# Kernel tuning notes

Hardware: AMD Instinct MI355X
Metric: run time of the kernel (lower is better)

Reference implementation:

```python
import jax, jax.numpy as jnp
import numpy as np

EPS = 1e-5


def _cbr(z, W, bn, relu=True):
    # z: [b, Cin, L]; W: [Cout, Cin]; bn: [4, Cout] = (gamma, beta, mean, var)
    # 1x1 Conv2d (bias=False) over a [b, Cin, L, 1] tensor == channel matmul.
    y = jnp.einsum('oi,bil->bol', W, z)
    g, b_, m, v = bn[0], bn[1], bn[2], bn[3]
    y = g[:, None] * (y - m[:, None]) * jax.lax.rsqrt(v[:, None] + EPS) + b_[:, None]
    return jax.nn.relu(y) if relu else y


def setup_inputs() -> dict:
    key = jax.random.key(0)
    ks = jax.random.split(key, 13)
    b, c, h, w = 32, 512, 48, 48
    in_spatial = h * w          # 2304
    inter_spatial = in_spatial // 4  # 576
    inter_channel = c // 4      # 128
    ncc = 1 + inter_channel     # 129
    return {
        'x': jax.random.normal(ks[0], (b, c, h, w), jnp.float32),
        'W_theta': jax.random.normal(ks[1], (inter_spatial, in_spatial), jnp.float32) * 0.02,
        'bn_theta': jax.random.uniform(ks[2], (4, inter_spatial), jnp.float32),
        'W_phi': jax.random.normal(ks[3], (inter_spatial, in_spatial), jnp.float32) * 0.02,
        'bn_phi': jax.random.uniform(ks[4], (4, inter_spatial), jnp.float32),
        'W_gx': jax.random.normal(ks[5], (inter_spatial, in_spatial), jnp.float32) * 0.02,
        'bn_gx': jax.random.uniform(ks[6], (4, inter_spatial), jnp.float32),
        'W_gg': jax.random.normal(ks[7], (inter_channel, 2 * c), jnp.float32) * 0.02,
        'bn_gg': jax.random.uniform(ks[8], (4, inter_channel), jnp.float32),
        'W_c1': jax.random.normal(ks[9], (ncc // 2, ncc), jnp.float32) * 0.02,
        'bn_c1': jax.random.uniform(ks[10], (4, ncc // 2), jnp.float32),
        'W_c2': jax.random.normal(ks[11], (1, ncc // 2), jnp.float32) * 0.02,
        'bn_c2': jax.random.uniform(ks[12], (4, 1), jnp.float32),
    }


def reference(x, W_theta, bn_theta, W_phi, bn_phi, W_gx, bn_gx,
              W_gg, bn_gg, W_c1, bn_c1, W_c2, bn_c2):
    b, c, h, w = x.shape
    xc = x.reshape(b, c, h * w).transpose(0, 2, 1)          # [b, hw, c]
    xc1 = _cbr(xc, W_theta, bn_theta).transpose(0, 2, 1)    # [b, c, is]
    xc2 = _cbr(xc, W_phi, bn_phi)                           # [b, is, c]
    Gc = jnp.einsum('bcs,bsd->bcd', xc1, xc2)               # [b, c, c]
    Gc_joint = jnp.concatenate([Gc.transpose(0, 2, 1), Gc], axis=1)  # [b, 2c, c]
    Gc_joint = _cbr(Gc_joint, W_gg, bn_gg)                  # [b, ic, c]
    g_xc = _cbr(xc, W_gx, bn_gx).mean(axis=1, keepdims=True)  # [b, 1, c]
    yc = jnp.concatenate([g_xc, Gc_joint], axis=1)          # [b, 1+ic, c]
    wy = _cbr(yc, W_c1, bn_c1)
    wy = _cbr(wy, W_c2, bn_c2, relu=False)                  # [b, 1, c]
    gate = jax.nn.sigmoid(wy)[:, 0, :, None, None]          # [b, c, 1, 1]
    return gate * x + x
```

## Files before the change

kernel.cpp:

```cpp
#include <hip/hip_runtime.h>
#include <cstdint>

#define EPSV 1e-5f
typedef unsigned short u16;
typedef __attribute__((ext_vector_type(8))) short bh8;
typedef __attribute__((ext_vector_type(4))) float f4;

__device__ __forceinline__ float bf2f(u16 h) { return __uint_as_float((unsigned)h << 16); }
__device__ __forceinline__ u16 f2bf(float x) {
    unsigned u = __float_as_uint(x);
    u += 0x7fffu + ((u >> 16) & 1u);
    return (u16)(u >> 16);
}

__device__ __forceinline__ void gl16(const void* g, const void* s) {
    __builtin_amdgcn_global_load_lds(
        reinterpret_cast<const __attribute__((address_space(1))) void*>((uintptr_t)g),
        reinterpret_cast<__attribute__((address_space(3))) void*>((unsigned)(uintptr_t)s),
        16, 0, 0);
}

__device__ __forceinline__ void core2(
    const u16* __restrict__ Ah, const u16* __restrict__ Al,
    const u16* __restrict__ Bh, const u16* __restrict__ Bl,
    long ldA, long ldB, int K, int rowA0, int rowB0,
    u16* lds, f4 acc[4][4])
{
    const int tid = threadIdx.x, l = tid & 63, w = tid >> 6;
    const int wr = w >> 1, wc = w & 1;
    const int srow = tid >> 2;
    const int schunk = ((tid & 3) ^ ((tid >> 3) & 3)) << 3;
    const size_t aoff = (size_t)(rowA0 + srow) * ldA + schunk;
    const size_t boff = (size_t)(rowB0 + srow) * ldB + schunk;
    const size_t a64 = (size_t)64 * ldA, b64 = (size_t)64 * ldB;
    const int rr = l & 15, cq = l >> 4;
    const int roff = rr * 64 + (((cq ^ ((rr >> 1) & 3))) << 4);
    char* const base0 = (char*)lds;
    char* const base1 = (char*)lds + 32768;
    const int nt = K >> 5;

#define STAGE_SWZ(base, s0) do { \
    gl16(Ah + aoff + (s0),       (base) +         w * 1024); \
    gl16(Ah + aoff + a64 + (s0), (base) +  4096 + w * 1024); \
    gl16(Al + aoff + (s0),       (base) +  8192 + w * 1024); \
    gl16(Al + aoff + a64 + (s0), (base) + 12288 + w * 1024); \
    gl16(Bh + boff + (s0),       (base) + 16384 + w * 1024); \
    gl16(Bh + boff + b64 + (s0), (base) + 20480 + w * 1024); \
    gl16(Bl + boff + (s0),       (base) + 24576 + w * 1024); \
    gl16(Bl + boff + b64 + (s0), (base) + 28672 + w * 1024); \
} while (0)

    STAGE_SWZ(base0, 0);
    __syncthreads();
    int p = 0;
    for (int t = 0; t < nt; ++t) {
        if (t + 1 < nt) STAGE_SWZ(p ? base0 : base1, (size_t)(t + 1) << 5);
        const char* buf = p ? base1 : base0;
        bh8 a_h[4], a_l[4], b_h[4], b_l[4];
#pragma unroll
        for (int i = 0; i < 4; ++i) {
            a_h[i] = *(const bh8*)(buf + (wr * 4 + i) * 1024 + roff);
            a_l[i] = *(const bh8*)(buf + 8192 + (wr * 4 + i) * 1024 + roff);
            b_h[i] = *(const bh8*)(buf + 16384 + (wc * 4 + i) * 1024 + roff);
            b_l[i] = *(const bh8*)(buf + 24576 + (wc * 4 + i) * 1024 + roff);
        }
#pragma unroll
        for (int i = 0; i < 4; ++i)
#pragma unroll
            for (int j = 0; j < 4; ++j)
                acc[i][j] = __builtin_amdgcn_mfma_f32_16x16x32_bf16(a_h[i], b_h[j], acc[i][j], 0, 0, 0);
#pragma unroll
        for (int i = 0; i < 4; ++i)
#pragma unroll
            for (int j = 0; j < 4; ++j)
                acc[i][j] = __builtin_amdgcn_mfma_f32_16x16x32_bf16(a_h[i], b_l[j], acc[i][j], 0, 0, 0);
#pragma unroll
        for (int i = 0; i < 4; ++i)
#pragma unroll
            for (int j = 0; j < 4; ++j)
                acc[i][j] = __builtin_amdgcn_mfma_f32_16x16x32_bf16(a_l[i], b_h[j], acc[i][j], 0, 0, 0);
        __syncthreads();
        p ^= 1;
    }
#undef STAGE_SWZ
}

__global__ __launch_bounds__(512) void gemm_s1_v6(
    const u16* __restrict__ Xh, const u16* __restrict__ Xl,
    const u16* __restrict__ W0h, const u16* __restrict__ W0l,
    const u16* __restrict__ W1h, const u16* __restrict__ W1l,
    const u16* __restrict__ W2h, const u16* __restrict__ W2l,
    const float* __restrict__ bn0, const float* __restrict__ bn1,
    const float* __restrict__ bn2,
    u16* __restrict__ Y0h, u16* __restrict__ Y0l,
    u16* __restrict__ Y1h, u16* __restrict__ Y1l,
    u16* __restrict__ Y2h, u16* __restrict__ Y2l)
{
    const int h = blockIdx.x;
    const int orig = (h & 7) * 120 + (h >> 3);
    const int ow = orig % 15;
    const int rest = orig / 15;
    const int ct = rest & 1, bz = rest >> 1;
    const int wi = ow / 5, otw = ow % 5;
    const bool full = (wi != 0);

    const u16* Bh = wi == 0 ? W0h : wi == 1 ? W1h : W2h;
    const u16* Bl = wi == 0 ? W0l : wi == 1 ? W1l : W2l;
    const float* bnp = wi == 0 ? bn0 : wi == 1 ? bn1 : bn2;
    u16* Yh = wi == 0 ? Y0h : wi == 1 ? Y1h : Y2h;
    u16* Yl = wi == 0 ? Y0l : wi == 1 ? Y1l : Y2l;

    __shared__ u16 lds[73728];

    const int tid = threadIdx.x, l = tid & 63, w = tid >> 6;
    const int wm = w >> 1, wn = w & 1;
    const int srow = tid >> 2;
    const int schunk = ((tid & 3) ^ ((tid >> 3) & 3)) << 3;
    const long ldK = 2304;
    const int rowA0 = bz * 512 + ct * 256;
    const int rowB0 = otw * 128;
    const size_t aoff = (size_t)(rowA0 + srow) * ldK + schunk;
    const size_t boff = (size_t)(rowB0 + srow) * ldK + schunk;
    const size_t a128 = (size_t)128 * ldK;
    const int rr = l & 15, cq = l >> 4;
    const int roff = rr * 64 + ((cq ^ ((rr >> 1) & 3)) << 4);
    char* const ldsb = (char*)lds;
    const int nt = 72;

#define ST_AHI(sb, s0) do { \
    gl16(Xh + aoff + (s0),        (sb) +         w * 1024); \
    gl16(Xh + aoff + a128 + (s0), (sb) +  8192 + w * 1024); } while (0)
#define ST_ALO(sb, s0) do { \
    gl16(Xl + aoff + (s0),        (sb) + 16384 + w * 1024); \
    gl16(Xl + aoff + a128 + (s0), (sb) + 24576 + w * 1024); } while (0)
#define ST_BHI(sb, s0) gl16(Bh + boff + (s0), (sb) + 32768 + w * 1024)
#define ST_BLO(sb, s0) gl16(Bl + boff + (s0), (sb) + 40960 + w * 1024)

    f4 acc[4][4];
    const f4 z4 = {0.f, 0.f, 0.f, 0.f};
#pragma unroll
    for (int i = 0; i < 4; ++i)
#pragma unroll
        for (int j = 0; j < 4; ++j) acc[i][j] = z4;

    ST_AHI(ldsb, 0); if (full) ST_ALO(ldsb, 0); ST_BHI(ldsb, 0); ST_BLO(ldsb, 0);
    ST_AHI(ldsb + 49152, 32); if (full) ST_ALO(ldsb + 49152, 32);
    ST_BHI(ldsb + 49152, 32); ST_BLO(ldsb + 49152, 32);
    if (full) asm volatile("s_waitcnt vmcnt(6)" ::: "memory");
    else      asm volatile("s_waitcnt vmcnt(4)" ::: "memory");
    __builtin_amdgcn_sched_barrier(0);
    __builtin_amdgcn_s_barrier();

    for (int t = 0; t < nt; ++t) {
        const char* buf = ldsb + (t % 3) * 49152;
        char* sbuf = ldsb + ((t + 2) % 3) * 49152;
        const bool pre = (t + 2 < nt);
        const int s0 = (t + 2) << 5;

        bh8 a_h[4], b_h[4], a_l[4], b_l[4];
#pragma unroll
        for (int i = 0; i < 4; ++i)
            a_h[i] = *(const bh8*)(buf + (wm * 4 + i) * 1024 + roff);
#pragma unroll
        for (int j = 0; j < 4; ++j)
            b_h[j] = *(const bh8*)(buf + 32768 + (wn * 4 + j) * 1024 + roff);
        if (pre) ST_AHI(sbuf, s0);
        __builtin_amdgcn_s_barrier();
        __builtin_amdgcn_s_setprio(1);
#pragma unroll
        for (int i = 0; i < 4; ++i)
#pragma unroll
            for (int j = 0; j < 4; ++j)
                acc[i][j] = __builtin_amdgcn_mfma_f32_16x16x32_bf16(a_h[i], b_h[j], acc[i][j], 0, 0, 0);
        __builtin_amdgcn_s_setprio(0);
        __builtin_amdgcn_s_barrier();
        if (full) {
#pragma unroll
            for (int i = 0; i < 4; ++i)
                a_l[i] = *(const bh8*)(buf + 16384 + (wm * 4 + i) * 1024 + roff);
        }
#pragma unroll
        for (int j = 0; j < 4; ++j)
            b_l[j] = *(const bh8*)(buf + 40960 + (wn * 4 + j) * 1024 + roff);
        if (pre) { if (full) ST_ALO(sbuf, s0); ST_BHI(sbuf, s0); }
        __builtin_amdgcn_s_barrier();
        __builtin_amdgcn_s_setprio(1);
#pragma unroll
        for (int i = 0; i < 4; ++i)
#pragma unroll
            for (int j = 0; j < 4; ++j)
                acc[i][j] = __builtin_amdgcn_mfma_f32_16x16x32_bf16(a_h[i], b_l[j], acc[i][j], 0, 0, 0);
        __builtin_amdgcn_s_setprio(0);
        __builtin_amdgcn_s_barrier();
        if (pre) ST_BLO(sbuf, s0);
        if (t + 1 < nt) {
            if (pre) {
                if (full) asm volatile("s_waitcnt vmcnt(6)" ::: "memory");
                else      asm volatile("s_waitcnt vmcnt(4)" ::: "memory");
            } else {
                asm volatile("s_waitcnt vmcnt(0)" ::: "memory");
            }
            __builtin_amdgcn_sched_barrier(0);
        }
        __builtin_amdgcn_s_barrier();
        if (full) {
            __builtin_amdgcn_s_setprio(1);
#pragma unroll
            for (int i = 0; i < 4; ++i)
#pragma unroll
                for (int j = 0; j < 4; ++j)
                    acc[i][j] = __builtin_amdgcn_mfma_f32_16x16x32_bf16(a_l[i], b_h[j], acc[i][j], 0, 0, 0);
            __builtin_amdgcn_s_setprio(0);
        }
        __builtin_amdgcn_s_barrier();
    }
#undef ST_AHI
#undef ST_ALO
#undef ST_BHI
#undef ST_BLO

    const int mb = ct * 256 + wm * 64;
    const int nbw = otw * 128 + wn * 64;
    const int lm = l & 15;
#pragma unroll
    for (int j = 0; j < 4; ++j) {
        const int o = nbw + j * 16 + lm;
        const bool val = (o < 576);
        float sc = 0.f, sh = 0.f;
        if (val) {
            const float gg = bnp[o], be = bnp[576 + o], mm = bnp[1152 + o], vv = bnp[1728 + o];
            sc = gg * rsqrtf(vv + EPSV);
            sh = be - mm * sc;
        }
#pragma unroll
        for (int i = 0; i < 4; ++i) {
            const int c = mb + i * 16 + ((l >> 4) << 2);
#pragma unroll
            for (int r = 0; r < 4; ++r) {
                const float y = val ? fmaxf(acc[i][j][r] * sc + sh, 0.f) : 0.f;
                const u16 hh = f2bf(y);
                const u16 lo = f2bf(y - bf2f(hh));
                const size_t off = ((size_t)bz * 512 + c + r) * 640 + o;
                Yh[off] = hh; Yl[off] = lo;
            }
        }
    }
}

__global__ __launch_bounds__(256) void gemm_u(
    const u16* __restrict__ Wggh, const u16* __restrict__ Wggl,
    const u16* __restrict__ tnth, const u16* __restrict__ tntl,
    const u16* __restrict__ pnth, const u16* __restrict__ pntl,
    u16* __restrict__ U1h, u16* __restrict__ U1l,
    u16* __restrict__ U2h, u16* __restrict__ U2l)
{
    const int h = blockIdx.x;
    const int orig = (h & 7) * 40 + (h >> 3);
    const int ot = orig % 5;
    const int rest = orig / 5;
    const int u = rest & 1, b = rest >> 1;

    const u16* Ah = Wggh + (u ? 512 : 0);
    const u16* Al = Wggl + (u ? 512 : 0);
    const u16* Bh = u ? tnth : pnth;
    const u16* Bl = u ? tntl : pntl;

    __shared__ u16 lds[32768];
    f4 acc[4][4];
    const f4 z4 = {0.f, 0.f, 0.f, 0.f};
#pragma unroll
    for (int i = 0; i < 4; ++i)
#pragma unroll
        for (int j = 0; j < 4; ++j) acc[i][j] = z4;

    core2(Ah, Al, Bh, Bl, 1024, 512, 512, 0, b * 640 + ot * 128, lds, acc);

    u16* Uh = u ? U2h : U1h;
    u16* Ul = u ? U2l : U1l;
    const int l = threadIdx.x & 63, w = threadIdx.x >> 6;
    const int wr = w >> 1, wc = w & 1;
#pragma unroll
    for (int i = 0; i < 4; ++i)
#pragma unroll
        for (int j = 0; j < 4; ++j)
#pragma unroll
            for (int r = 0; r < 4; ++r) {
                const int irow = wr * 64 + i * 16 + ((l >> 4) << 2) + r;
                const int ocol = ot * 128 + wc * 64 + j * 16 + (l & 15);
                const float v = acc[i][j][r];
                const u16 hh = f2bf(v);
                const u16 lo = f2bf(v - bf2f(hh));
                const size_t off = ((size_t)b * 128 + irow) * 640 + ocol;
                Uh[off] = hh; Ul[off] = lo;
            }
}

__global__ __launch_bounds__(256) void gemm_term_p(
    const u16* __restrict__ U1h, const u16* __restrict__ U1l,
    const u16* __restrict__ U2h, const u16* __restrict__ U2l,
    const u16* __restrict__ tth, const u16* __restrict__ ttl,
    const u16* __restrict__ pth, const u16* __restrict__ ptl,
    float* __restrict__ GGa, float* __restrict__ GGb)
{
    const int h = blockIdx.x;
    const int orig = (h & 7) * 32 + (h >> 3);
    const int dt = orig & 3;
    const int u = (orig >> 2) & 1;
    const int b = orig >> 3;

    const u16* Ah = u ? U2h : U1h;
    const u16* Al = u ? U2l : U1l;
    const u16* Bh = u ? pth : tth;
    const u16* Bl = u ? ptl : ttl;
    float* G = u ? GGb : GGa;

    __shared__ u16 lds[32768];
    f4 acc[4][4];
    const f4 z4 = {0.f, 0.f, 0.f, 0.f};
#pragma unroll
    for (int i = 0; i < 4; ++i)
#pragma unroll
        for (int j = 0; j < 4; ++j) acc[i][j] = z4;

    core2(Ah, Al, Bh, Bl, 640, 640, 640,
          b * 128, b * 512 + dt * 128, lds, acc);

    const int l = threadIdx.x & 63, w = threadIdx.x >> 6;
    const int wr = w >> 1, wc = w & 1;
#pragma unroll
    for (int i = 0; i < 4; ++i)
#pragma unroll
        for (int j = 0; j < 4; ++j)
#pragma unroll
            for (int r = 0; r < 4; ++r) {
                const int irow = wr * 64 + i * 16 + ((l >> 4) << 2) + r;
                const int dcol = dt * 128 + wc * 64 + j * 16 + (l & 15);
                G[((size_t)b * 128 + irow) * 512 + dcol] = acc[i][j][r];
            }
}

__global__ __launch_bounds__(256) void gg_combine(
    float* __restrict__ GGa, const float* __restrict__ GGb,
    const float* __restrict__ bn, long n4)
{
    const long i = (long)blockIdx.x * 256 + threadIdx.x;
    if (i >= n4) return;
    const int irow = (int)((i >> 7) & 127);
    const float g = bn[irow], be = bn[128 + irow], m = bn[256 + irow], v = bn[384 + irow];
    const float sc = g * rsqrtf(v + EPSV);
    const float sh = be - m * sc;
    float4 a = ((const float4*)GGa)[i];
    const float4 b = ((const float4*)GGb)[i];
    a.x = fmaxf((a.x + b.x) * sc + sh, 0.f);
    a.y = fmaxf((a.y + b.y) * sc + sh, 0.f);
    a.z = fmaxf((a.z + b.z) * sc + sh, 0.f);
    a.w = fmaxf((a.w + b.w) * sc + sh, 0.f);
    ((float4*)GGa)[i] = a;
}

__global__ __launch_bounds__(256) void transpose_y(
    const u16* __restrict__ s0, u16* __restrict__ d0,
    const u16* __restrict__ s1, u16* __restrict__ d1,
    const u16* __restrict__ s2, u16* __restrict__ d2,
    const u16* __restrict__ s3, u16* __restrict__ d3)
{
    const int pz = blockIdx.z;
    const int b = pz >> 2, pl = pz & 3;
    const u16* src = pl == 0 ? s0 : pl == 1 ? s1 : pl == 2 ? s2 : s3;
    u16* dst = pl == 0 ? d0 : pl == 1 ? d1 : pl == 2 ? d2 : d3;
    const int o0 = blockIdx.x * 64, c0 = blockIdx.y * 64;
    __shared__ u16 t[64][72];
    const int tid = threadIdx.x;
#pragma unroll
    for (int rdx = tid; rdx < 512; rdx += 256) {
        const int c = rdx >> 3, oc = (rdx & 7) << 3;
        *(bh8*)&t[c][oc] = *(const bh8*)&src[((size_t)b * 512 + c0 + c) * 640 + o0 + oc];
    }
    __syncthreads();
#pragma unroll
    for (int wdx = tid; wdx < 512; wdx += 256) {
        const int o = wdx >> 3, cc = (wdx & 7) << 3;
        u16 v[8];
#pragma unroll
        for (int e = 0; e < 8; ++e) v[e] = t[cc + e][o];
        *(bh8*)&dst[((size_t)b * 640 + o0 + o) * 512 + c0 + cc] = *(bh8*)&v[0];
    }
}

__global__ __launch_bounds__(256) void conv_split(
    const float* __restrict__ in, u16* __restrict__ hi, u16* __restrict__ lo, long n8)
{
    long i = (long)blockIdx.x * 256 + threadIdx.x;
    const long stride = (long)gridDim.x * 256;
    for (; i < n8; i += stride) {
        const float4 a = ((const float4*)in)[2 * i];
        const float4 b = ((const float4*)in)[2 * i + 1];
        const float v[8] = {a.x, a.y, a.z, a.w, b.x, b.y, b.z, b.w};
        unsigned hw[4], lw[4];
#pragma unroll
        for (int k = 0; k < 4; ++k) {
            const u16 h0 = f2bf(v[2 * k]), h1 = f2bf(v[2 * k + 1]);
            const u16 l0 = f2bf(v[2 * k] - bf2f(h0)), l1 = f2bf(v[2 * k + 1] - bf2f(h1));
            hw[k] = (unsigned)h0 | ((unsigned)h1 << 16);
            lw[k] = (unsigned)l0 | ((unsigned)l1 << 16);
        }
        *(uint4*)&hi[8 * i] = make_uint4(hw[0], hw[1], hw[2], hw[3]);
        *(uint4*)&lo[8 * i] = make_uint4(lw[0], lw[1], lw[2], lw[3]);
    }
}

__global__ __launch_bounds__(256) void conv_w_pad(
    const float* __restrict__ W, u16* __restrict__ hi, u16* __restrict__ lo,
    int rows, long n8)
{
    const long i = (long)blockIdx.x * 256 + threadIdx.x;
    if (i >= n8) return;
    const long e = i * 8;
    const int row = (int)(e / 2304);
    unsigned hw[4] = {0, 0, 0, 0}, lw[4] = {0, 0, 0, 0};
    if (row < rows) {
        const float4 a = ((const float4*)W)[2 * i];
        const float4 b = ((const float4*)W)[2 * i + 1];
        const float v[8] = {a.x, a.y, a.z, a.w, b.x, b.y, b.z, b.w};
#pragma unroll
        for (int k = 0; k < 4; ++k) {
            const u16 h0 = f2bf(v[2 * k]), h1 = f2bf(v[2 * k + 1]);
            const u16 l0 = f2bf(v[2 * k] - bf2f(h0)), l1 = f2bf(v[2 * k + 1] - bf2f(h1));
            hw[k] = (unsigned)h0 | ((unsigned)h1 << 16);
            lw[k] = (unsigned)l0 | ((unsigned)l1 << 16);
        }
    }
    *(uint4*)&hi[8 * i] = make_uint4(hw[0], hw[1], hw[2], hw[3]);
    *(uint4*)&lo[8 * i] = make_uint4(lw[0], lw[1], lw[2], lw[3]);
}

__global__ __launch_bounds__(256) void row_mean(
    const u16* __restrict__ Yh, const u16* __restrict__ Yl,
    float* __restrict__ out, int rows)
{
    const int l = threadIdx.x & 63;
    const int row = blockIdx.x * 4 + (threadIdx.x >> 6);
    if (row >= rows) return;
    const u16* ph = Yh + (size_t)row * 640;
    const u16* pl = Yl + (size_t)row * 640;
    float s = 0.f;
    struct U8 { u16 u[8]; };
    for (int k = l; k < 80; k += 64) {
        const U8 a = *(const U8*)&ph[k * 8];
        const U8 b = *(const U8*)&pl[k * 8];
#pragma unroll
        for (int e = 0; e < 8; ++e) s += bf2f(a.u[e]) + bf2f(b.u[e]);
    }
    for (int off = 32; off; off >>= 1) s += __shfl_down(s, off, 64);
    if (l == 0) out[row] = s * (1.f / 576.f);
}

__global__ __launch_bounds__(256)
void gate_kernel(const float* __restrict__ gxc, const float* __restrict__ GG,
                 const float* __restrict__ Wc1, const float* __restrict__ bn1,
                 const float* __restrict__ Wc2, const float* __restrict__ bn2,
                 float* __restrict__ gate, int IC, int D, int OC)
{
    const int b  = blockIdx.y;
    const int d0 = blockIdx.x * 64;

    __shared__ float yc_s[129][64];
    __shared__ float part[4][64];

    const int tid = threadIdx.x;
    for (int idx = tid; idx < 129 * 64; idx += 256) {
        const int j = idx >> 6, d = idx & 63;
        yc_s[j][d] = (j == 0) ? gxc[b * D + d0 + d]
                              : GG[((size_t)b * IC + (j - 1)) * D + d0 + d];
    }
    __syncthreads();

    const int d = tid & 63;
    const int q = tid >> 6;
    float acc2 = 0.f;
    for (int o = q * 16; o < q * 16 + 16; ++o) {
        float s = 0.f;
        const float* __restrict__ w = &Wc1[o * 129];
        for (int j = 0; j < 129; ++j) s = fmaf(w[j], yc_s[j][d], s);
        const float g1 = bn1[o], be1 = bn1[OC + o], m1 = bn1[2 * OC + o], v1 = bn1[3 * OC + o];
        const float sc = g1 / sqrtf(v1 + EPSV);
        const float w1 = fmaxf(s * sc + (be1 - m1 * sc), 0.f);
        acc2 = fmaf(Wc2[o], w1, acc2);
    }
    part[q][d] = acc2;
    __syncthreads();
    if (q == 0) {
        const float s = part[0][d] + part[1][d] + part[2][d] + part[3][d];
        const float g2 = bn2[0], be2 = bn2[1], m2 = bn2[2], v2 = bn2[3];
        const float sc = g2 / sqrtf(v2 + EPSV);
        const float wy = s * sc + (be2 - m2 * sc);
        gate[b * D + d0 + d] = 1.f / (1.f + expf(-wy));
    }
}

__global__ __launch_bounds__(256)
void final_kernel(const float* __restrict__ x, const float* __restrict__ gate,
                  float* __restrict__ out, long n4, int sp4)
{
    long i = (long)blockIdx.x * blockDim.x + threadIdx.x;
    const long stride = (long)gridDim.x * blockDim.x;
    for (; i < n4; i += stride) {
        float4 v = ((const float4*)x)[i];
        const long bc = i / sp4;
        const float gm = 1.f + gate[bc];
        v.x *= gm; v.y *= gm; v.z *= gm; v.w *= gm;
        ((float4*)out)[i] = v;
    }
}

extern "C" void kernel_launch(void* const* d_in, const int* in_sizes, int n_in,
                              void* d_out, int out_size, void* d_ws, size_t ws_size,
                              hipStream_t stream)
{
    const float* x        = (const float*)d_in[0];
    const float* W_theta  = (const float*)d_in[1];
    const float* bn_theta = (const float*)d_in[2];
    const float* W_phi    = (const float*)d_in[3];
    const float* bn_phi   = (const float*)d_in[4];
    const float* W_gx     = (const float*)d_in[5];
    const float* bn_gx    = (const float*)d_in[6];
    const float* W_gg     = (const float*)d_in[7];
    const float* bn_gg    = (const float*)d_in[8];
    const float* W_c1     = (const float*)d_in[9];
    const float* bn_c1    = (const float*)d_in[10];
    const float* W_c2     = (const float*)d_in[11];
    const float* bn_c2    = (const float*)d_in[12];
    float* out = (float*)d_out;

    const int B = 32, C = 512, S = 2304, O = 576, OP = 640, IC = 128, OC = 64;
    const size_t P  = (size_t)B * C * OP;
    const size_t WP = (size_t)OP * S;
    const size_t UP = (size_t)B * IC * OP;

    u16* tth = (u16*)d_out;
    u16* ttl = tth + P;
    u16* pth = ttl + P;
    u16* ptl = pth + P;
    u16* Wgh = ptl + P;
    u16* Wgl = Wgh + WP;
    u16* Wth = Wgl + WP;
    u16* Wtl = Wth + WP;
    u16* Wph = Wtl + WP;
    u16* Wpl = Wph + WP;
    u16* wggh = Wpl + WP;
    u16* wggl = wggh + (size_t)IC * 1024;
    u16* u1h = wggl + (size_t)IC * 1024;
    u16* u1l = u1h + UP;
    u16* u2h = u1l + UP;
    u16* u2l = u2h + UP;
    float* GGa = (float*)(u2l + UP);
    float* GGb = GGa + (size_t)B * IC * C;

    u16* Xhi  = (u16*)d_ws;
    u16* Xlo  = Xhi + (size_t)B * C * S;
    u16* ygxh = Xlo + (size_t)B * C * S;
    u16* ygxl = ygxh + P;
    float* gxc  = (float*)(ygxl + P);
    float* gate = gxc + (size_t)B * C;
    u16* tnth = (u16*)d_ws;
    u16* tntl = tnth + P;
    u16* pnth = tntl + P;
    u16* pntl = pnth + P;

    const dim3 blk(256);

    const long wN8 = (long)WP / 8;
    conv_w_pad<<<dim3((unsigned)(wN8 / 256)), blk, 0, stream>>>(W_gx,    Wgh, Wgl, O, wN8);
    conv_w_pad<<<dim3((unsigned)(wN8 / 256)), blk, 0, stream>>>(W_theta, Wth, Wtl, O, wN8);
    conv_w_pad<<<dim3((unsigned)(wN8 / 256)), blk, 0, stream>>>(W_phi,   Wph, Wpl, O, wN8);
    conv_split<<<dim3(64), blk, 0, stream>>>(W_gg, wggh, wggl, (long)IC * 1024 / 8);

    conv_split<<<dim3(2048), blk, 0, stream>>>(x, Xhi, Xlo, (long)B * C * S / 8);
    gemm_s1_v6<<<dim3(960), dim3(512), 0, stream>>>(
        Xhi, Xlo, Wgh, Wgl, Wth, Wtl, Wph, Wpl,
        bn_gx, bn_theta, bn_phi,
        ygxh, ygxl, tth, ttl, pth, ptl);
    row_mean<<<dim3(4096), blk, 0, stream>>>(ygxh, ygxl, gxc, B * C);

    transpose_y<<<dim3(10, 8, 128), blk, 0, stream>>>(
        tth, tnth, ttl, tntl, pth, pnth, ptl, pntl);

    gemm_u<<<dim3(320), blk, 0, stream>>>(wggh, wggl, tnth, tntl, pnth, pntl,
                                          u1h, u1l, u2h, u2l);

    gemm_term_p<<<dim3(256), blk, 0, stream>>>(u1h, u1l, u2h, u2l,
                                               tth, ttl, pth, ptl, GGa, GGb);
    gg_combine<<<dim3(2048), blk, 0, stream>>>(GGa, GGb, bn_gg,
                                               (long)B * IC * C / 4);

    gate_kernel<<<dim3(C / 64, B), blk, 0, stream>>>(gxc, GGa, W_c1, bn_c1, W_c2, bn_c2,
                                                     gate, IC, C, OC);

    final_kernel<<<dim3(2048), blk, 0, stream>>>(x, gate, out,
                                                 (long)B * C * S / 4, S / 4);
}
```

Measured before the change: 633.2 us.

## Fuse fp32-to-bf16 hi/lo split of x into the stage-1 GEMM loads

Drops the separate conv_split pass over x and has the stage-1 GEMM stream fp32 x straight into LDS. Each tile is split into bf16 hi/lo pairs in registers right after the LDS read. This removes one full read and two half-size writes of the 151 MB input, plus a kernel launch. In exchange the GEMM moves twice the A bytes per tile (fp32 instead of bf16), and every block redundantly recomputes the split. The non-full (wi==0) blocks now also load the low-part data volume.

```diff
diff --git a/kernel.cpp b/kernel.cpp
--- a/kernel.cpp
+++ b/kernel.cpp
@@ -18,6 +18,25 @@
         reinterpret_cast<const __attribute__((address_space(1))) void*>((uintptr_t)g),
         reinterpret_cast<__attribute__((address_space(3))) void*>((unsigned)(uintptr_t)s),
         16, 0, 0);
+}
+
+__device__ __forceinline__ void split8(const f4 va, const f4 vb,
+                                       bh8* hi, bh8* lo, bool needLo)
+{
+    union U { bh8 v; u16 u[8]; };
+    U H, L;
+#pragma unroll
+    for (int e = 0; e < 4; ++e) {
+        const float x0 = va[e], x1 = vb[e];
+        const u16 h0 = f2bf(x0), h1 = f2bf(x1);
+        H.u[e] = h0; H.u[e + 4] = h1;
+        if (needLo) {
+            L.u[e]     = f2bf(x0 - bf2f(h0));
+            L.u[e + 4] = f2bf(x1 - bf2f(h1));
+        }
+    }
+    *hi = H.v;
+    if (needLo) *lo = L.v;
 }
 
 __device__ __forceinline__ void core2(
@@ -85,8 +104,8 @@
 #undef STAGE_SWZ
 }
 
-__global__ __launch_bounds__(512) void gemm_s1_v6(
-    const u16* __restrict__ Xh, const u16* __restrict__ Xl,
+__global__ __launch_bounds__(512) void gemm_s1_v7(
+    const float* __restrict__ Xf,
     const u16* __restrict__ W0h, const u16* __restrict__ W0l,
     const u16* __restrict__ W1h, const u16* __restrict__ W1l,
     const u16* __restrict__ W2h, const u16* __restrict__ W2l,
@@ -114,25 +133,30 @@
 
     const int tid = threadIdx.x, l = tid & 63, w = tid >> 6;
     const int wm = w >> 1, wn = w & 1;
-    const int srow = tid >> 2;
-    const int schunk = ((tid & 3) ^ ((tid >> 3) & 3)) << 3;
     const long ldK = 2304;
     const int rowA0 = bz * 512 + ct * 256;
     const int rowB0 = otw * 128;
-    const size_t aoff = (size_t)(rowA0 + srow) * ldK + schunk;
+
+    const int arow = tid >> 3;
+    const int acd  = (tid & 7) ^ (arow & 7);
+    const size_t aoffF = (size_t)(rowA0 + arow) * ldK + acd * 4;
+    const int srow = tid >> 2;
+    const int schunk = ((tid & 3) ^ ((tid >> 3) & 3)) << 3;
     const size_t boff = (size_t)(rowB0 + srow) * ldK + schunk;
-    const size_t a128 = (size_t)128 * ldK;
+
     const int rr = l & 15, cq = l >> 4;
-    const int roff = rr * 64 + ((cq ^ ((rr >> 1) & 3)) << 4);
+    const int roffB = rr * 64 + ((cq ^ ((rr >> 1) & 3)) << 4);
+    const int slot1 = (2 * cq) ^ (rr & 7);
+    const int roffA1 = rr * 128 + (slot1 << 4);
+    const int roffA2 = rr * 128 + ((slot1 ^ 1) << 4);
     char* const ldsb = (char*)lds;
     const int nt = 72;
 
-#define ST_AHI(sb, s0) do { \
-    gl16(Xh + aoff + (s0),        (sb) +         w * 1024); \
-    gl16(Xh + aoff + a128 + (s0), (sb) +  8192 + w * 1024); } while (0)
-#define ST_ALO(sb, s0) do { \
-    gl16(Xl + aoff + (s0),        (sb) + 16384 + w * 1024); \
-    gl16(Xl + aoff + a128 + (s0), (sb) + 24576 + w * 1024); } while (0)
+#define ST_A(sb, s0) do { \
+    gl16(Xf + aoffF + (s0),          (sb) +         w * 1024); \
+    gl16(Xf + aoffF + 147456 + (s0), (sb) +  8192 + w * 1024); \
+    gl16(Xf + aoffF + 294912 + (s0), (sb) + 16384 + w * 1024); \
+    gl16(Xf + aoffF + 442368 + (s0), (sb) + 24576 + w * 1024); } while (0)
 #define ST_BHI(sb, s0) gl16(Bh + boff + (s0), (sb) + 32768 + w * 1024)
 #define ST_BLO(sb, s0) gl16(Bl + boff + (s0), (sb) + 40960 + w * 1024)
 
@@ -143,11 +167,9 @@
 #pragma unroll
         for (int j = 0; j < 4; ++j) acc[i][j] = z4;
 
-    ST_AHI(ldsb, 0); if (full) ST_ALO(ldsb, 0); ST_BHI(ldsb, 0); ST_BLO(ldsb, 0);
-    ST_AHI(ldsb + 49152, 32); if (full) ST_ALO(ldsb + 49152, 32);
-    ST_BHI(ldsb + 49152, 32); ST_BLO(ldsb + 49152, 32);
-    if (full) asm volatile("s_waitcnt vmcnt(6)" ::: "memory");
-    else      asm volatile("s_waitcnt vmcnt(4)" ::: "memory");
+    ST_A(ldsb, 0); ST_BHI(ldsb, 0); ST_BLO(ldsb, 0);
+    ST_A(ldsb + 49152, 32); ST_BHI(ldsb + 49152, 32); ST_BLO(ldsb + 49152, 32);
+    asm volatile("s_waitcnt vmcnt(6)" ::: "memory");
     __builtin_amdgcn_sched_barrier(0);
     __builtin_amdgcn_s_barrier();
 
@@ -157,14 +179,18 @@
         const bool pre = (t + 2 < nt);
         const int s0 = (t + 2) << 5;
 
-        bh8 a_h[4], b_h[4], a_l[4], b_l[4];
-#pragma unroll
-        for (int i = 0; i < 4; ++i)
-            a_h[i] = *(const bh8*)(buf + (wm * 4 + i) * 1024 + roff);
+        if (pre) ST_A(sbuf, s0);
+        bh8 a_h[4], a_l[4], b_h[4], b_l[4];
+#pragma unroll
+        for (int i = 0; i < 4; ++i) {
+            const int fb = (wm * 64 + i * 16) * 128;
+            const f4 va = *(const f4*)(buf + fb + roffA1);
+            const f4 vb = *(const f4*)(buf + fb + roffA2);
+            split8(va, vb, &a_h[i], &a_l[i], full);
+        }
 #pragma unroll
         for (int j = 0; j < 4; ++j)
-            b_h[j] = *(const bh8*)(buf + 32768 + (wn * 4 + j) * 1024 + roff);
-        if (pre) ST_AHI(sbuf, s0);
+            b_h[j] = *(const bh8*)(buf + 32768 + (wn * 4 + j) * 1024 + roffB);
         __builtin_amdgcn_s_barrier();
         __builtin_amdgcn_s_setprio(1);
 #pragma unroll
@@ -174,15 +200,10 @@
                 acc[i][j] = __builtin_amdgcn_mfma_f32_16x16x32_bf16(a_h[i], b_h[j], acc[i][j], 0, 0, 0);
         __builtin_amdgcn_s_setprio(0);
         __builtin_amdgcn_s_barrier();
-        if (full) {
-#pragma unroll
-            for (int i = 0; i < 4; ++i)
-                a_l[i] = *(const bh8*)(buf + 16384 + (wm * 4 + i) * 1024 + roff);
-        }
+        if (pre) ST_BHI(sbuf, s0);
 #pragma unroll
         for (int j = 0; j < 4; ++j)
-            b_l[j] = *(const bh8*)(buf + 40960 + (wn * 4 + j) * 1024 + roff);
-        if (pre) { if (full) ST_ALO(sbuf, s0); ST_BHI(sbuf, s0); }
+            b_l[j] = *(const bh8*)(buf + 40960 + (wn * 4 + j) * 1024 + roffB);
         __builtin_amdgcn_s_barrier();
         __builtin_amdgcn_s_setprio(1);
 #pragma unroll
@@ -194,12 +215,8 @@
         __builtin_amdgcn_s_barrier();
         if (pre) ST_BLO(sbuf, s0);
         if (t + 1 < nt) {
-            if (pre) {
-                if (full) asm volatile("s_waitcnt vmcnt(6)" ::: "memory");
-                else      asm volatile("s_waitcnt vmcnt(4)" ::: "memory");
-            } else {
-                asm volatile("s_waitcnt vmcnt(0)" ::: "memory");
-            }
+            if (pre) asm volatile("s_waitcnt vmcnt(6)" ::: "memory");
+            else     asm volatile("s_waitcnt vmcnt(0)" ::: "memory");
             __builtin_amdgcn_sched_barrier(0);
         }
         __builtin_amdgcn_s_barrier();
@@ -214,8 +231,7 @@
         }
         __builtin_amdgcn_s_barrier();
     }
-#undef ST_AHI
-#undef ST_ALO
+#undef ST_A
 #undef ST_BHI
 #undef ST_BLO
 
@@ -556,16 +572,14 @@
     float* GGa = (float*)(u2l + UP);
     float* GGb = GGa + (size_t)B * IC * C;
 
-    u16* Xhi  = (u16*)d_ws;
-    u16* Xlo  = Xhi + (size_t)B * C * S;
-    u16* ygxh = Xlo + (size_t)B * C * S;
-    u16* ygxl = ygxh + P;
-    float* gxc  = (float*)(ygxl + P);
-    float* gate = gxc + (size_t)B * C;
     u16* tnth = (u16*)d_ws;
     u16* tntl = tnth + P;
     u16* pnth = tntl + P;
     u16* pntl = pnth + P;
+    u16* ygxh = pntl + P;
+    u16* ygxl = ygxh + P;
+    float* gxc  = (float*)(ygxl + P);
+    float* gate = gxc + (size_t)B * C;
 
     const dim3 blk(256);
 
@@ -575,9 +589,8 @@
     conv_w_pad<<<dim3((unsigned)(wN8 / 256)), blk, 0, stream>>>(W_phi,   Wph, Wpl, O, wN8);
     conv_split<<<dim3(64), blk, 0, stream>>>(W_gg, wggh, wggl, (long)IC * 1024 / 8);
 
-    conv_split<<<dim3(2048), blk, 0, stream>>>(x, Xhi, Xlo, (long)B * C * S / 8);
-    gemm_s1_v6<<<dim3(960), dim3(512), 0, stream>>>(
-        Xhi, Xlo, Wgh, Wgl, Wth, Wtl, Wph, Wpl,
+    gemm_s1_v7<<<dim3(960), dim3(512), 0, stream>>>(
+        x, Wgh, Wgl, Wth, Wtl, Wph, Wpl,
         bn_gx, bn_theta, bn_phi,
         ygxh, ygxl, tth, ttl, pth, ptl);
     row_mean<<<dim3(4096), blk, 0, stream>>>(ygxh, ygxl, gxc, B * C);
```

New measurement: 908.9 us. +43.5%, slower.

## Fuse g_x row mean into GEMM epilogue and gg_combine into gate kernel

Applied to the files above, without the earlier changes.

The g_x branch of the big GEMM now reduces its BN+ReLU output across the tile's output columns in registers and LDS and writes per-tile partial row sums, instead of storing the full hi/lo bf16 matrix and running a separate row_mean kernel. The GGa+GGb combine with BN+ReLU moves into gate_kernel's load loop, which also sums the five partial means. The three weight conversion launches are merged into one 2D grid. This removes a large intermediate write/read and several launches, at the cost of extra epilogue syncs and shuffles in the GEMM.

```diff
diff --git a/kernel.cpp b/kernel.cpp
--- a/kernel.cpp
+++ b/kernel.cpp
@@ -85,14 +85,14 @@
 #undef STAGE_SWZ
 }
 
-__global__ __launch_bounds__(512) void gemm_s1_v6(
+__global__ __launch_bounds__(512) void gemm_s1_v6b(
     const u16* __restrict__ Xh, const u16* __restrict__ Xl,
     const u16* __restrict__ W0h, const u16* __restrict__ W0l,
     const u16* __restrict__ W1h, const u16* __restrict__ W1l,
     const u16* __restrict__ W2h, const u16* __restrict__ W2l,
     const float* __restrict__ bn0, const float* __restrict__ bn1,
     const float* __restrict__ bn2,
-    u16* __restrict__ Y0h, u16* __restrict__ Y0l,
+    float* __restrict__ gxc_part,
     u16* __restrict__ Y1h, u16* __restrict__ Y1l,
     u16* __restrict__ Y2h, u16* __restrict__ Y2l)
 {
@@ -107,23 +107,23 @@
     const u16* Bh = wi == 0 ? W0h : wi == 1 ? W1h : W2h;
     const u16* Bl = wi == 0 ? W0l : wi == 1 ? W1l : W2l;
     const float* bnp = wi == 0 ? bn0 : wi == 1 ? bn1 : bn2;
-    u16* Yh = wi == 0 ? Y0h : wi == 1 ? Y1h : Y2h;
-    u16* Yl = wi == 0 ? Y0l : wi == 1 ? Y1l : Y2l;
+    u16* Yh = wi == 1 ? Y1h : Y2h;
+    u16* Yl = wi == 1 ? Y1l : Y2l;
 
     __shared__ u16 lds[73728];
 
     const int tid = threadIdx.x, l = tid & 63, w = tid >> 6;
     const int wm = w >> 1, wn = w & 1;
-    const int srow = tid >> 2;
-    const int schunk = ((tid & 3) ^ ((tid >> 3) & 3)) << 3;
     const long ldK = 2304;
     const int rowA0 = bz * 512 + ct * 256;
     const int rowB0 = otw * 128;
+    const int srow = tid >> 2;
+    const int schunk = ((tid & 3) ^ ((tid >> 3) & 3)) << 3;
     const size_t aoff = (size_t)(rowA0 + srow) * ldK + schunk;
     const size_t boff = (size_t)(rowB0 + srow) * ldK + schunk;
     const size_t a128 = (size_t)128 * ldK;
-    const int rr = l & 15, cq = l >> 4;
-    const int roff = rr * 64 + ((cq ^ ((rr >> 1) & 3)) << 4);
+    const int rr = l & 15, cq2 = l >> 4;
+    const int roff = rr * 64 + ((cq2 ^ ((rr >> 1) & 3)) << 4);
     char* const ldsb = (char*)lds;
     const int nt = 72;
 
@@ -221,27 +221,66 @@
 
     const int mb = ct * 256 + wm * 64;
     const int nbw = otw * 128 + wn * 64;
-    const int lm = l & 15;
-#pragma unroll
-    for (int j = 0; j < 4; ++j) {
-        const int o = nbw + j * 16 + lm;
-        const bool val = (o < 576);
-        float sc = 0.f, sh = 0.f;
-        if (val) {
-            const float gg = bnp[o], be = bnp[576 + o], mm = bnp[1152 + o], vv = bnp[1728 + o];
-            sc = gg * rsqrtf(vv + EPSV);
-            sh = be - mm * sc;
-        }
-#pragma unroll
-        for (int i = 0; i < 4; ++i) {
-            const int c = mb + i * 16 + ((l >> 4) << 2);
+    const int lm = l & 15, cq = l >> 4;
+
+    if (wi == 0) {
+        float rs[4][4] = {};
+#pragma unroll
+        for (int j = 0; j < 4; ++j) {
+            const int o = nbw + j * 16 + lm;
+            const bool val = (o < 576);
+            float sc = 0.f, sh = 0.f;
+            if (val) {
+                const float gg = bnp[o], be = bnp[576 + o], mm = bnp[1152 + o], vv = bnp[1728 + o];
+                sc = gg * rsqrtf(vv + EPSV);
+                sh = be - mm * sc;
+            }
+#pragma unroll
+            for (int i = 0; i < 4; ++i)
+#pragma unroll
+                for (int r = 0; r < 4; ++r)
+                    rs[i][r] += val ? fmaxf(acc[i][j][r] * sc + sh, 0.f) : 0.f;
+        }
+        __syncthreads();
+        float* ldsF = (float*)lds;
+#pragma unroll
+        for (int i = 0; i < 4; ++i)
 #pragma unroll
             for (int r = 0; r < 4; ++r) {
-                const float y = val ? fmaxf(acc[i][j][r] * sc + sh, 0.f) : 0.f;
-                const u16 hh = f2bf(y);
-                const u16 lo = f2bf(y - bf2f(hh));
-                const size_t off = ((size_t)bz * 512 + c + r) * 640 + o;
-                Yh[off] = hh; Yl[off] = lo;
+                float v = rs[i][r];
+                v += __shfl_xor(v, 1, 64);
+                v += __shfl_xor(v, 2, 64);
+                v += __shfl_xor(v, 4, 64);
+                v += __shfl_xor(v, 8, 64);
+                if (lm == 0)
+                    ldsF[wn * 256 + wm * 64 + i * 16 + cq * 4 + r] = v;
+            }
+        __syncthreads();
+        if (tid < 256)
+            gxc_part[(size_t)otw * 16384 + (size_t)bz * 512 + ct * 256 + tid]
+                = ldsF[tid] + ldsF[256 + tid];
+    } else {
+#pragma unroll
+        for (int j = 0; j < 4; ++j) {
+            const int o = nbw + j * 16 + lm;
+            const bool val = (o < 576);
+            float sc = 0.f, sh = 0.f;
+            if (val) {
+                const float gg = bnp[o], be = bnp[576 + o], mm = bnp[1152 + o], vv = bnp[1728 + o];
+                sc = gg * rsqrtf(vv + EPSV);
+                sh = be - mm * sc;
+            }
+#pragma unroll
+            for (int i = 0; i < 4; ++i) {
+                const int c = mb + i * 16 + (cq << 2);
+#pragma unroll
+                for (int r = 0; r < 4; ++r) {
+                    const float y = val ? fmaxf(acc[i][j][r] * sc + sh, 0.f) : 0.f;
+                    const u16 hh = f2bf(y);
+                    const u16 lo = f2bf(y - bf2f(hh));
+                    const size_t off = ((size_t)bz * 512 + c + r) * 640 + o;
+                    Yh[off] = hh; Yl[off] = lo;
+                }
             }
         }
     }
@@ -339,25 +378,6 @@
             }
 }
 
-__global__ __launch_bounds__(256) void gg_combine(
-    float* __restrict__ GGa, const float* __restrict__ GGb,
-    const float* __restrict__ bn, long n4)
-{
-    const long i = (long)blockIdx.x * 256 + threadIdx.x;
-    if (i >= n4) return;
-    const int irow = (int)((i >> 7) & 127);
-    const float g = bn[irow], be = bn[128 + irow], m = bn[256 + irow], v = bn[384 + irow];
-    const float sc = g * rsqrtf(v + EPSV);
-    const float sh = be - m * sc;
-    float4 a = ((const float4*)GGa)[i];
-    const float4 b = ((const float4*)GGb)[i];
-    a.x = fmaxf((a.x + b.x) * sc + sh, 0.f);
-    a.y = fmaxf((a.y + b.y) * sc + sh, 0.f);
-    a.z = fmaxf((a.z + b.z) * sc + sh, 0.f);
-    a.w = fmaxf((a.w + b.w) * sc + sh, 0.f);
-    ((float4*)GGa)[i] = a;
-}
-
 __global__ __launch_bounds__(256) void transpose_y(
     const u16* __restrict__ s0, u16* __restrict__ d0,
     const u16* __restrict__ s1, u16* __restrict__ d1,
@@ -409,10 +429,19 @@
     }
 }
 
-__global__ __launch_bounds__(256) void conv_w_pad(
-    const float* __restrict__ W, u16* __restrict__ hi, u16* __restrict__ lo,
+__global__ __launch_bounds__(256) void conv_w_pad3(
+    const float* __restrict__ Wg, const float* __restrict__ Wt,
+    const float* __restrict__ Wp,
+    u16* __restrict__ Hg, u16* __restrict__ Lg,
+    u16* __restrict__ Ht, u16* __restrict__ Lt,
+    u16* __restrict__ Hp, u16* __restrict__ Lp,
     int rows, long n8)
 {
+    const int wsel = blockIdx.y;
+    const float* W = wsel == 0 ? Wg : wsel == 1 ? Wt : Wp;
+    u16* hi = wsel == 0 ? Hg : wsel == 1 ? Ht : Hp;
+    u16* lo = wsel == 0 ? Lg : wsel == 1 ? Lt : Lp;
+
     const long i = (long)blockIdx.x * 256 + threadIdx.x;
     if (i >= n8) return;
     const long e = i * 8;
@@ -434,29 +463,10 @@
     *(uint4*)&lo[8 * i] = make_uint4(lw[0], lw[1], lw[2], lw[3]);
 }
 
-__global__ __launch_bounds__(256) void row_mean(
-    const u16* __restrict__ Yh, const u16* __restrict__ Yl,
-    float* __restrict__ out, int rows)
-{
-    const int l = threadIdx.x & 63;
-    const int row = blockIdx.x * 4 + (threadIdx.x >> 6);
-    if (row >= rows) return;
-    const u16* ph = Yh + (size_t)row * 640;
-    const u16* pl = Yl + (size_t)row * 640;
-    float s = 0.f;
-    struct U8 { u16 u[8]; };
-    for (int k = l; k < 80; k += 64) {
-        const U8 a = *(const U8*)&ph[k * 8];
-        const U8 b = *(const U8*)&pl[k * 8];
-#pragma unroll
-        for (int e = 0; e < 8; ++e) s += bf2f(a.u[e]) + bf2f(b.u[e]);
-    }
-    for (int off = 32; off; off >>= 1) s += __shfl_down(s, off, 64);
-    if (l == 0) out[row] = s * (1.f / 576.f);
-}
-
 __global__ __launch_bounds__(256)
-void gate_kernel(const float* __restrict__ gxc, const float* __restrict__ GG,
+void gate_kernel(const float* __restrict__ gxp,
+                 const float* __restrict__ GGa, const float* __restrict__ GGb,
+                 const float* __restrict__ bngg,
                  const float* __restrict__ Wc1, const float* __restrict__ bn1,
                  const float* __restrict__ Wc2, const float* __restrict__ bn2,
                  float* __restrict__ gate, int IC, int D, int OC)
@@ -470,8 +480,23 @@
     const int tid = threadIdx.x;
     for (int idx = tid; idx < 129 * 64; idx += 256) {
         const int j = idx >> 6, d = idx & 63;
-        yc_s[j][d] = (j == 0) ? gxc[b * D + d0 + d]
-                              : GG[((size_t)b * IC + (j - 1)) * D + d0 + d];
+        float v;
+        if (j == 0) {
+            float s = 0.f;
+#pragma unroll
+            for (int t = 0; t < 5; ++t)
+                s += gxp[(size_t)t * 16384 + (size_t)b * 512 + d0 + d];
+            v = s * (1.f / 576.f);
+        } else {
+            const int i = j - 1;
+            const float g = bngg[i], be = bngg[128 + i];
+            const float m = bngg[256 + i], vv = bngg[384 + i];
+            const float sc = g * rsqrtf(vv + EPSV);
+            const float sh = be - m * sc;
+            const size_t o = ((size_t)b * IC + i) * D + d0 + d;
+            v = fmaxf((GGa[o] + GGb[o]) * sc + sh, 0.f);
+        }
+        yc_s[j][d] = v;
     }
     __syncthreads();
 
@@ -558,29 +583,25 @@
 
     u16* Xhi  = (u16*)d_ws;
     u16* Xlo  = Xhi + (size_t)B * C * S;
-    u16* ygxh = Xlo + (size_t)B * C * S;
-    u16* ygxl = ygxh + P;
-    float* gxc  = (float*)(ygxl + P);
-    float* gate = gxc + (size_t)B * C;
     u16* tnth = (u16*)d_ws;
     u16* tntl = tnth + P;
     u16* pnth = tntl + P;
     u16* pntl = pnth + P;
+    float* gxc_part = (float*)(Xlo + (size_t)B * C * S);
+    float* gate = gxc_part + (size_t)5 * B * C;
 
     const dim3 blk(256);
 
     const long wN8 = (long)WP / 8;
-    conv_w_pad<<<dim3((unsigned)(wN8 / 256)), blk, 0, stream>>>(W_gx,    Wgh, Wgl, O, wN8);
-    conv_w_pad<<<dim3((unsigned)(wN8 / 256)), blk, 0, stream>>>(W_theta, Wth, Wtl, O, wN8);
-    conv_w_pad<<<dim3((unsigned)(wN8 / 256)), blk, 0, stream>>>(W_phi,   Wph, Wpl, O, wN8);
+    conv_w_pad3<<<dim3((unsigned)(wN8 / 256), 3), blk, 0, stream>>>(
+        W_gx, W_theta, W_phi, Wgh, Wgl, Wth, Wtl, Wph, Wpl, O, wN8);
     conv_split<<<dim3(64), blk, 0, stream>>>(W_gg, wggh, wggl, (long)IC * 1024 / 8);
 
     conv_split<<<dim3(2048), blk, 0, stream>>>(x, Xhi, Xlo, (long)B * C * S / 8);
-    gemm_s1_v6<<<dim3(960), dim3(512), 0, stream>>>(
+    gemm_s1_v6b<<<dim3(960), dim3(512), 0, stream>>>(
         Xhi, Xlo, Wgh, Wgl, Wth, Wtl, Wph, Wpl,
         bn_gx, bn_theta, bn_phi,
-        ygxh, ygxl, tth, ttl, pth, ptl);
-    row_mean<<<dim3(4096), blk, 0, stream>>>(ygxh, ygxl, gxc, B * C);
+        gxc_part, tth, ttl, pth, ptl);
 
     transpose_y<<<dim3(10, 8, 128), blk, 0, stream>>>(
         tth, tnth, ttl, tntl, pth, pnth, ptl, pntl);
@@ -590,11 +611,10 @@
 
     gemm_term_p<<<dim3(256), blk, 0, stream>>>(u1h, u1l, u2h, u2l,
                                                tth, ttl, pth, ptl, GGa, GGb);
-    gg_combine<<<dim3(2048), blk, 0, stream>>>(GGa, GGb, bn_gg,
-                                               (long)B * IC * C / 4);
-
-    gate_kernel<<<dim3(C / 64, B), blk, 0, stream>>>(gxc, GGa, W_c1, bn_c1, W_c2, bn_c2,
-                                                     gate, IC, C, OC);
+
+    gate_kernel<<<dim3(C / 64, B), blk, 0, stream>>>(
+        gxc_part, GGa, GGb, bn_gg, W_c1, bn_c1, W_c2, bn_c2,
+        gate, IC, C, OC);
 
     final_kernel<<<dim3(2048), blk, 0, stream>>>(x, gate, out,
                                                  (long)B * C * S / 4, S / 4);
```

Measured after the change: 611.1 us, median of 2. 1.04x faster.
